# Kernel optimization log

Measured on AMD Instinct MI355X. Metric: run time of the kernel, lower is better.

The kernel has to match this reference:

```python
import jax, jax.numpy as jnp
import numpy as np

N_NODES = 50000
N_EDGES = 1600000
NFEAT = 128
NHID = 128
NCLASS = 64
BATCH = 8


def setup_inputs() -> dict:
    key = jax.random.key(0)
    ks = jax.random.split(key, 8)
    x = jax.random.normal(ks[0], (BATCH, N_NODES, NFEAT), dtype=jnp.float32)
    edge_rows = jnp.sort(jax.random.randint(ks[1], (N_EDGES,), 0, N_NODES))
    edge_cols = jax.random.randint(ks[2], (N_EDGES,), 0, N_NODES)
    # roughly degree-normalized positive weights (avg degree 32)
    edge_vals = jax.random.uniform(ks[3], (N_EDGES,), dtype=jnp.float32) / 32.0
    s1 = 1.0 / np.sqrt(NFEAT)
    W1 = jax.random.normal(ks[4], (NFEAT, NHID), dtype=jnp.float32) * s1
    W2 = jax.random.normal(ks[5], (NHID, NHID), dtype=jnp.float32) * s1
    W3 = jax.random.normal(ks[6], (NHID, NCLASS), dtype=jnp.float32) * s1
    b1 = jnp.zeros((NHID,), dtype=jnp.float32)
    b2 = jnp.zeros((NHID,), dtype=jnp.float32)
    b3 = jnp.zeros((NCLASS,), dtype=jnp.float32)
    return {"x": x, "edge_rows": edge_rows, "edge_cols": edge_cols,
            "edge_vals": edge_vals, "W1": W1, "b1": b1, "W2": W2,
            "b2": b2, "W3": W3, "b3": b3}


def _gcn_layer(x, W, b, rows, cols, vals, n_nodes):
    """Batched SPGraphConvolution: spmm(adj, x @ W) + b, x: [B, N, d_in]."""
    support = jnp.einsum("bnd,de->bne", x, W)  # [B, N, d_out]

    def spmm(s):  # s: [N, d_out]
        msgs = s[cols] * vals[:, None]  # gather + scale, [E, d_out]
        return jax.ops.segment_sum(msgs, rows, num_segments=n_nodes)

    return jax.vmap(spmm)(support) + b


def reference(x, edge_rows, edge_cols, edge_vals, W1, b1, W2, b2, W3, b3):
    n = x.shape[1]
    # dropout in eval mode (training=False) for determinism
    h = jax.nn.relu(_gcn_layer(x, W1, b1, edge_rows, edge_cols, edge_vals, n) + x)
    h = jax.nn.relu(_gcn_layer(h, W2, b2, edge_rows, edge_cols, edge_vals, n) + h)
    h = jax.nn.relu(_gcn_layer(h, W3, b3, edge_rows, edge_cols, edge_vals, n))
    return jax.nn.sigmoid(h)
```

## Files before the change

kernel.cpp:

```cpp
#include <hip/hip_runtime.h>

constexpr int NN = 50000;
constexpr int NE = 1600000;
constexpr int NB = 8;
constexpr int M_ROWS = NN * NB;

typedef unsigned short ushort;
typedef unsigned int uint;
typedef unsigned char uchar;
typedef float f32x2v __attribute__((ext_vector_type(2)));
typedef float f32x4v __attribute__((ext_vector_type(4)));
typedef uint u32x4 __attribute__((ext_vector_type(4)));
typedef uint u32x2 __attribute__((ext_vector_type(2)));

__device__ __forceinline__ ushort f2bf(float f) {
  union { float f; uint u; } v;
  v.f = f;
  const uint r = v.u + 0x7fffu + ((v.u >> 16) & 1u);
  return (ushort)(r >> 16);
}
__device__ __forceinline__ float bfhi(uint g) {
  union { uint u; float f; } v;
  v.u = g & 0xffff0000u;
  return v.f;
}
__device__ __forceinline__ float bflo(uint g) {
  union { uint u; float f; } v;
  v.u = g << 16;
  return v.f;
}

__device__ __forceinline__ void fp8x4_to_f32x2(uint v, f32x2v& lo, f32x2v& hi) {
#if __has_builtin(__builtin_amdgcn_cvt_pk_f32_fp8)
  lo = __builtin_amdgcn_cvt_pk_f32_fp8((int)v, false);
  hi = __builtin_amdgcn_cvt_pk_f32_fp8((int)v, true);
#else
  union { _Float16 h; ushort u; } c0, c1, c2, c3;
  c0.u = (ushort)(((v & 0x80u) << 8) | ((v & 0x7fu) << 7));
  c1.u = (ushort)(((v & 0x8000u)) | ((v & 0x7f00u) >> 1));
  c2.u = (ushort)((((v >> 16) & 0x80u) << 8) | (((v >> 16) & 0x7fu) << 7));
  c3.u = (ushort)((((v >> 24) & 0x80u) << 8) | (((v >> 24) & 0x7fu) << 7));
  lo.x = (float)c0.h * 256.0f;
  lo.y = (float)c1.h * 256.0f;
  hi.x = (float)c2.h * 256.0f;
  hi.y = (float)c3.h * 256.0f;
#endif
}
__device__ __forceinline__ uint f32_to_fp8(float x) {
#if __has_builtin(__builtin_amdgcn_cvt_pk_fp8_f32)
  return (uint)__builtin_amdgcn_cvt_pk_fp8_f32(x, x, 0, false) & 0xffu;
#else
  union { _Float16 h; ushort u; } c;
  c.h = (_Float16)(x * (1.0f / 256.0f));
  const uint h = c.u;
  uint r = h & 0x7fffu;
  r = (r + 0x3Fu + ((r >> 7) & 1u)) >> 7;
  if (r > 0x7Eu) r = 0x7Eu;
  return ((h >> 8) & 0x80u) | r;
#endif
}

__global__ __launch_bounds__(256) void rowptr_kernel(const int* __restrict__ rows,
                                                     int* __restrict__ row_ptr) {
  const int r = blockIdx.x * 256 + threadIdx.x;
  if (r > NN) return;
  int lo = 0, hi = NE;
  while (lo < hi) {
    const int mid = (lo + hi) >> 1;
    if (rows[mid] < r) lo = mid + 1;
    else hi = mid;
  }
  row_ptr[r] = lo;
}

__global__ __launch_bounds__(256) void wtrans_kernel(const float* __restrict__ W,
                                                     ushort* __restrict__ Wt,
                                                     int dout) {
  const int idx = blockIdx.x * 256 + threadIdx.x;
  if (idx >= dout * 128) return;
  const int n = idx >> 7;
  const int k = idx & 127;
  Wt[idx] = f2bf(W[k * dout + n]);
}

template <int DOUT, bool ABF16>
__global__ __launch_bounds__(256) void gemm_mfma(const void* __restrict__ Av,
                                                 const ushort* __restrict__ Wt,
                                                 uchar* __restrict__ S) {
  constexpr int PACK = 256 / DOUT;
  constexpr int NT = DOUT / 16;
  constexpr int RT = 5;
  constexpr int LDK = 136;
  constexpr int LB = DOUT + 16;
  typedef __attribute__((ext_vector_type(8))) short bf16x8;
  typedef __attribute__((ext_vector_type(4))) float f32x4;

  __shared__ ushort As[64 * LDK];
  __shared__ ushort Ws[DOUT * LDK];

  const int t = threadIdx.x;
  const int w = t >> 6;
  const int l = t & 63;

#pragma unroll
  for (int q = 0; q < (DOUT * 128) / (8 * 256); q++) {
    const int chunk = t + q * 256;
    const int n = chunk >> 4;
    const int off = (chunk & 15) * 8;
    *(uint4*)(Ws + n * LDK + off) = *(const uint4*)(Wt + n * 128 + off);
  }

  const int mrow = w * 16 + (l & 15);
  const int q8 = (l >> 4) * 8;

  for (int rt = 0; rt < RT; rt++) {
    const size_t m0 = (size_t)blockIdx.x * (64 * RT) + (size_t)rt * 64;

    if constexpr (ABF16) {
      const ushort* A = (const ushort*)Av;
#pragma unroll
      for (int q = 0; q < 4; q++) {
        const int chunk = t + q * 256;
        const int row = chunk >> 4;
        const int off = (chunk & 15) * 8;
        *(u32x4*)(As + row * LDK + off) =
            __builtin_nontemporal_load((const u32x4*)(A + (m0 + row) * 128 + off));
      }
    } else {
      const float* A = (const float*)Av;
      const int row = t >> 2;
      const int c0 = (t & 3) * 32;
      const float* src = A + (m0 + row) * 128 + c0;
      ushort* dst = As + row * LDK + c0;
#pragma unroll
      for (int q = 0; q < 8; q++) {
        const f32x4v g = __builtin_nontemporal_load((const f32x4v*)(src + q * 4));
        u32x2 p;
        p.x = (uint)f2bf(g.x) | ((uint)f2bf(g.y) << 16);
        p.y = (uint)f2bf(g.z) | ((uint)f2bf(g.w) << 16);
        *(u32x2*)(dst + q * 4) = p;
      }
    }
    __syncthreads();

    bf16x8 a[4];
    const ushort* ap = As + mrow * LDK + q8;
#pragma unroll
    for (int ks = 0; ks < 4; ks++) a[ks] = *(const bf16x8*)(ap + ks * 32);

    f32x4 acc[NT];
#pragma unroll
    for (int nt = 0; nt < NT; nt++) acc[nt] = (f32x4)0.f;

#pragma unroll
    for (int nt = 0; nt < NT; nt++) {
      const ushort* bp = Ws + (nt * 16 + (l & 15)) * LDK + q8;
#pragma unroll
      for (int ks = 0; ks < 4; ks++) {
        const bf16x8 b = *(const bf16x8*)(bp + ks * 32);
        acc[nt] =
            __builtin_amdgcn_mfma_f32_16x16x32_bf16(a[ks], b, acc[nt], 0, 0, 0);
      }
    }

    __syncthreads();
    uchar* Ab = (uchar*)As;
    const int erow = w * 16 + (l >> 4) * 4;
    const int ecol = l & 15;
#pragma unroll
    for (int nt = 0; nt < NT; nt++)
#pragma unroll
      for (int r = 0; r < 4; r++)
        Ab[(erow + r) * LB + nt * 16 + ecol] = (uchar)f32_to_fp8(acc[nt][r]);
    __syncthreads();

#pragma unroll
    for (int q = 0; q < (64 * DOUT) / (16 * 256); q++) {
      const int chunk = t + q * 256;
      const int row = chunk / (DOUT / 16);
      const int off = (chunk % (DOUT / 16)) * 16;
      const uint4 v = *(const uint4*)(Ab + row * LB + off);
      const int m = (int)m0 + row;
      const int b = m / NN;
      const int n = m - b * NN;
      *(uint4*)(S + ((size_t)(b / PACK) * NN + n) * 256 + (b % PACK) * DOUT + off) = v;
    }
    __syncthreads();
  }
}

template <int PACK, int RMODE, bool SIGMOID, bool OBF16>
__global__ __launch_bounds__(256) void spmm_kernel(
    const uchar* __restrict__ S, const int* __restrict__ row_ptr,
    const int* __restrict__ cols, const float* __restrict__ vals,
    const float* __restrict__ bias, const void* resid, void* out) {
  constexpr int DOUT = 256 / PACK;
  constexpr int LPB = 64 / PACK;

  const int wave = threadIdx.x >> 6;
  const int lane = threadIdx.x & 63;
  const int r = __builtin_amdgcn_readfirstlane(blockIdx.x * 4 + wave);
  const int bg = lane / LPB;
  const int j = (lane % LPB) * 4;
  const int b = blockIdx.y * PACK + bg;
  const uchar* __restrict__ Sg = S + (size_t)blockIdx.y * ((size_t)NN * 256);
  const uint lane4 = (uint)lane << 2;

  f32x2v a01 = {0.f, 0.f};
  f32x2v a23 = {0.f, 0.f};

  const int e0 = __builtin_amdgcn_readfirstlane(row_ptr[r]);
  const int e1 = __builtin_amdgcn_readfirstlane(row_ptr[r + 1]);

  int e = e0;
  for (; e + 16 <= e1; e += 16) {
    uint gg[16];
#pragma unroll
    for (int s = 0; s < 16; s++) {
      const uint c8 = ((uint)cols[e + s]) << 8;
      gg[s] = *(const uint*)(Sg + c8 + lane4);
    }
#pragma unroll
    for (int s = 0; s < 16; s++) {
      const float wi = vals[e + s];
      f32x2v lo, hi;
      fp8x4_to_f32x2(gg[s], lo, hi);
      const f32x2v w2 = {wi, wi};
      a01 = __builtin_elementwise_fma(w2, lo, a01);
      a23 = __builtin_elementwise_fma(w2, hi, a23);
    }
  }
  for (; e + 4 <= e1; e += 4) {
    uint gg[4];
#pragma unroll
    for (int s = 0; s < 4; s++) {
      const uint c8 = ((uint)cols[e + s]) << 8;
      gg[s] = *(const uint*)(Sg + c8 + lane4);
    }
#pragma unroll
    for (int s = 0; s < 4; s++) {
      const float wi = vals[e + s];
      f32x2v lo, hi;
      fp8x4_to_f32x2(gg[s], lo, hi);
      const f32x2v w2 = {wi, wi};
      a01 = __builtin_elementwise_fma(w2, lo, a01);
      a23 = __builtin_elementwise_fma(w2, hi, a23);
    }
  }
  for (; e < e1; e++) {
    const uint c8 = ((uint)cols[e]) << 8;
    const float wi = vals[e];
    const uint g = *(const uint*)(Sg + c8 + lane4);
    f32x2v lo, hi;
    fp8x4_to_f32x2(g, lo, hi);
    const f32x2v w2 = {wi, wi};
    a01 = __builtin_elementwise_fma(w2, lo, a01);
    a23 = __builtin_elementwise_fma(w2, hi, a23);
  }

  float a0 = a01.x, a1 = a01.y, a2 = a23.x, a3 = a23.y;

  const size_t orow = (size_t)(b * NN + r) * DOUT + j;
  const f32x4v bb = *(const f32x4v*)(bias + j);
  a0 += bb.x;
  a1 += bb.y;
  a2 += bb.z;
  a3 += bb.w;
  if constexpr (RMODE == 1) {
    const f32x4v res =
        __builtin_nontemporal_load((const f32x4v*)((const float*)resid + orow));
    a0 += res.x;
    a1 += res.y;
    a2 += res.z;
    a3 += res.w;
  } else if constexpr (RMODE == 2) {
    const u32x2 g =
        __builtin_nontemporal_load((const u32x2*)((const ushort*)resid + orow));
    a0 += bflo(g.x);
    a1 += bfhi(g.x);
    a2 += bflo(g.y);
    a3 += bfhi(g.y);
  }
  a0 = fmaxf(a0, 0.f);
  a1 = fmaxf(a1, 0.f);
  a2 = fmaxf(a2, 0.f);
  a3 = fmaxf(a3, 0.f);
  if constexpr (SIGMOID) {
    a0 = 1.f / (1.f + __expf(-a0));
    a1 = 1.f / (1.f + __expf(-a1));
    a2 = 1.f / (1.f + __expf(-a2));
    a3 = 1.f / (1.f + __expf(-a3));
  }
  if constexpr (OBF16) {
    u32x2 o;
    o.x = (uint)f2bf(a0) | ((uint)f2bf(a1) << 16);
    o.y = (uint)f2bf(a2) | ((uint)f2bf(a3) << 16);
    __builtin_nontemporal_store(o, (u32x2*)((ushort*)out + orow));
  } else {
    f32x4v o;
    o.x = a0;
    o.y = a1;
    o.z = a2;
    o.w = a3;
    __builtin_nontemporal_store(o, (f32x4v*)((float*)out + orow));
  }
}

extern "C" void kernel_launch(void* const* d_in, const int* in_sizes, int n_in,
                              void* d_out, int out_size, void* d_ws, size_t ws_size,
                              hipStream_t stream) {
  const float* x = (const float*)d_in[0];
  const int* erows = (const int*)d_in[1];
  const int* ecols = (const int*)d_in[2];
  const float* evals = (const float*)d_in[3];
  const float* W1 = (const float*)d_in[4];
  const float* b1 = (const float*)d_in[5];
  const float* W2 = (const float*)d_in[6];
  const float* b2 = (const float*)d_in[7];
  const float* W3 = (const float*)d_in[8];
  const float* b3 = (const float*)d_in[9];

  char* ws = (char*)d_ws;
  int* row_ptr = (int*)ws;
  ushort* Wt1 = (ushort*)(ws + 0x40000);
  ushort* Wt2 = (ushort*)(ws + 0x48000);
  ushort* Wt3 = (ushort*)(ws + 0x50000);
  uchar* Sf8 = (uchar*)(ws + 0x60000);
  ushort* H = (ushort*)(ws + 0x60000 + (size_t)M_ROWS * 128);

  rowptr_kernel<<<(NN + 256) / 256, 256, 0, stream>>>(erows, row_ptr);
  wtrans_kernel<<<(128 * 128) / 256, 256, 0, stream>>>(W1, Wt1, 128);
  wtrans_kernel<<<(128 * 128) / 256, 256, 0, stream>>>(W2, Wt2, 128);
  wtrans_kernel<<<(64 * 128) / 256, 256, 0, stream>>>(W3, Wt3, 64);

  const dim3 sgrid128(NN / 4, NB / 2);
  const dim3 sgrid64(NN / 4, NB / 4);
  constexpr int GB = M_ROWS / (64 * 5);

  gemm_mfma<128, false><<<GB, 256, 0, stream>>>(x, Wt1, Sf8);
  spmm_kernel<2, 1, false, true><<<sgrid128, 256, 0, stream>>>(
      Sf8, row_ptr, ecols, evals, b1, x, H);
  gemm_mfma<128, true><<<GB, 256, 0, stream>>>(H, Wt2, Sf8);
  spmm_kernel<2, 2, false, true><<<sgrid128, 256, 0, stream>>>(
      Sf8, row_ptr, ecols, evals, b2, H, H);
  gemm_mfma<64, true><<<GB, 256, 0, stream>>>(H, Wt3, Sf8);
  spmm_kernel<4, 0, true, false><<<sgrid64, 256, 0, stream>>>(
      Sf8, row_ptr, ecols, evals, b3, nullptr, (float*)d_out);
}
```

Before: 930.4 us.

## Store fp8 support in 64-byte column slabs and split edges across wave quarters

The GEMM now writes the fp8 support matrix as column slabs of 64 bytes per node instead of 256-byte packed rows. The SpMM is restructured so each wave's four 16-lane quarters handle different edges of the same row, using vector loads of cols and vals, and the partial sums are combined with cross-lane shuffles. Blocks are ordered so that 8 slices are processed in phases, aiming to keep each slab's working set (about 3.2 MB) resident in cache and to raise memory-level parallelism. The costs are more launched blocks, repeated reads of row_ptr, cols and vals once per slice, and shuffle overhead.

```diff
diff --git a/kernel.cpp b/kernel.cpp
--- a/kernel.cpp
+++ b/kernel.cpp
@@ -4,6 +4,7 @@
 constexpr int NE = 1600000;
 constexpr int NB = 8;
 constexpr int M_ROWS = NN * NB;
+constexpr int SLAB = NN * 64;
 
 typedef unsigned short ushort;
 typedef unsigned int uint;
@@ -12,6 +13,8 @@
 typedef float f32x4v __attribute__((ext_vector_type(4)));
 typedef uint u32x4 __attribute__((ext_vector_type(4)));
 typedef uint u32x2 __attribute__((ext_vector_type(2)));
+typedef uint u32x4a __attribute__((ext_vector_type(4), aligned(4)));
+typedef float f32x4a __attribute__((ext_vector_type(4), aligned(4)));
 
 __device__ __forceinline__ ushort f2bf(float f) {
   union { float f; uint u; } v;
@@ -87,7 +90,6 @@
 __global__ __launch_bounds__(256) void gemm_mfma(const void* __restrict__ Av,
                                                  const ushort* __restrict__ Wt,
                                                  uchar* __restrict__ S) {
-  constexpr int PACK = 256 / DOUT;
   constexpr int NT = DOUT / 16;
   constexpr int RT = 5;
   constexpr int LDK = 136;
@@ -183,28 +185,34 @@
       const int m = (int)m0 + row;
       const int b = m / NN;
       const int n = m - b * NN;
-      *(uint4*)(S + ((size_t)(b / PACK) * NN + n) * 256 + (b % PACK) * DOUT + off) = v;
+      const int gcol = b * DOUT + off;
+      *(uint4*)(S + (size_t)(gcol >> 6) * SLAB + (size_t)n * 64 + (gcol & 63)) = v;
     }
     __syncthreads();
   }
 }
 
-template <int PACK, int RMODE, bool SIGMOID, bool OBF16>
-__global__ __launch_bounds__(256) void spmm_kernel(
+template <int SLICES, int SPB, int RMODE, bool SIGMOID, bool OBF16>
+__global__ __launch_bounds__(256) void spmm_sliced(
     const uchar* __restrict__ S, const int* __restrict__ row_ptr,
     const int* __restrict__ cols, const float* __restrict__ vals,
     const float* __restrict__ bias, const void* resid, void* out) {
-  constexpr int DOUT = 256 / PACK;
-  constexpr int LPB = 64 / PACK;
+  constexpr int D = SPB * 64;
+  constexpr int PER_PHASE = (NN / 4) * 8;
 
   const int wave = threadIdx.x >> 6;
   const int lane = threadIdx.x & 63;
-  const int r = __builtin_amdgcn_readfirstlane(blockIdx.x * 4 + wave);
-  const int bg = lane / LPB;
-  const int j = (lane % LPB) * 4;
-  const int b = blockIdx.y * PACK + bg;
-  const uchar* __restrict__ Sg = S + (size_t)blockIdx.y * ((size_t)NN * 256);
-  const uint lane4 = (uint)lane << 2;
+  const int q = lane >> 4;
+  const int qi = lane & 15;
+
+  const int bid = blockIdx.x;
+  const int phase = bid / PER_PHASE;
+  const int within = bid - phase * PER_PHASE;
+  const int slice = phase * 8 + (within & 7);
+  const int rc = within >> 3;
+  const int r = __builtin_amdgcn_readfirstlane(rc * 4 + wave);
+
+  const uint vbase = (uint)slice * (uint)SLAB + (uint)(qi * 4);
 
   f32x2v a01 = {0.f, 0.f};
   f32x2v a23 = {0.f, 0.f};
@@ -214,95 +222,101 @@
 
   int e = e0;
   for (; e + 16 <= e1; e += 16) {
-    uint gg[16];
-#pragma unroll
-    for (int s = 0; s < 16; s++) {
-      const uint c8 = ((uint)cols[e + s]) << 8;
-      gg[s] = *(const uint*)(Sg + c8 + lane4);
-    }
-#pragma unroll
-    for (int s = 0; s < 16; s++) {
-      const float wi = vals[e + s];
+    const int eq = e + q * 4;
+    const u32x4a cc = *(const u32x4a*)(cols + eq);
+    const f32x4a ww = *(const f32x4a*)(vals + eq);
+    uint g0 = *(const uint*)(S + ((cc.x << 6) + vbase));
+    uint g1 = *(const uint*)(S + ((cc.y << 6) + vbase));
+    uint g2 = *(const uint*)(S + ((cc.z << 6) + vbase));
+    uint g3 = *(const uint*)(S + ((cc.w << 6) + vbase));
+    f32x2v lo, hi;
+    fp8x4_to_f32x2(g0, lo, hi);
+    f32x2v w2 = {ww.x, ww.x};
+    a01 = __builtin_elementwise_fma(w2, lo, a01);
+    a23 = __builtin_elementwise_fma(w2, hi, a23);
+    fp8x4_to_f32x2(g1, lo, hi);
+    w2.x = ww.y; w2.y = ww.y;
+    a01 = __builtin_elementwise_fma(w2, lo, a01);
+    a23 = __builtin_elementwise_fma(w2, hi, a23);
+    fp8x4_to_f32x2(g2, lo, hi);
+    w2.x = ww.z; w2.y = ww.z;
+    a01 = __builtin_elementwise_fma(w2, lo, a01);
+    a23 = __builtin_elementwise_fma(w2, hi, a23);
+    fp8x4_to_f32x2(g3, lo, hi);
+    w2.x = ww.w; w2.y = ww.w;
+    a01 = __builtin_elementwise_fma(w2, lo, a01);
+    a23 = __builtin_elementwise_fma(w2, hi, a23);
+  }
+  if (e < e1) {
+    const int eqt = e + q * 4;
+#pragma unroll
+    for (int k = 0; k < 4; k++) {
+      const int idx = eqt + k;
+      const int cidx = idx < e1 ? idx : e1 - 1;
+      const uint cv = (uint)cols[cidx];
+      const float wk = idx < e1 ? vals[cidx] : 0.f;
+      const uint g = *(const uint*)(S + ((cv << 6) + vbase));
       f32x2v lo, hi;
-      fp8x4_to_f32x2(gg[s], lo, hi);
-      const f32x2v w2 = {wi, wi};
+      fp8x4_to_f32x2(g, lo, hi);
+      const f32x2v w2 = {wk, wk};
       a01 = __builtin_elementwise_fma(w2, lo, a01);
       a23 = __builtin_elementwise_fma(w2, hi, a23);
     }
   }
-  for (; e + 4 <= e1; e += 4) {
-    uint gg[4];
-#pragma unroll
-    for (int s = 0; s < 4; s++) {
-      const uint c8 = ((uint)cols[e + s]) << 8;
-      gg[s] = *(const uint*)(Sg + c8 + lane4);
-    }
-#pragma unroll
-    for (int s = 0; s < 4; s++) {
-      const float wi = vals[e + s];
-      f32x2v lo, hi;
-      fp8x4_to_f32x2(gg[s], lo, hi);
-      const f32x2v w2 = {wi, wi};
-      a01 = __builtin_elementwise_fma(w2, lo, a01);
-      a23 = __builtin_elementwise_fma(w2, hi, a23);
-    }
-  }
-  for (; e < e1; e++) {
-    const uint c8 = ((uint)cols[e]) << 8;
-    const float wi = vals[e];
-    const uint g = *(const uint*)(Sg + c8 + lane4);
-    f32x2v lo, hi;
-    fp8x4_to_f32x2(g, lo, hi);
-    const f32x2v w2 = {wi, wi};
-    a01 = __builtin_elementwise_fma(w2, lo, a01);
-    a23 = __builtin_elementwise_fma(w2, hi, a23);
-  }
 
   float a0 = a01.x, a1 = a01.y, a2 = a23.x, a3 = a23.y;
-
-  const size_t orow = (size_t)(b * NN + r) * DOUT + j;
-  const f32x4v bb = *(const f32x4v*)(bias + j);
-  a0 += bb.x;
-  a1 += bb.y;
-  a2 += bb.z;
-  a3 += bb.w;
-  if constexpr (RMODE == 1) {
-    const f32x4v res =
-        __builtin_nontemporal_load((const f32x4v*)((const float*)resid + orow));
-    a0 += res.x;
-    a1 += res.y;
-    a2 += res.z;
-    a3 += res.w;
-  } else if constexpr (RMODE == 2) {
-    const u32x2 g =
-        __builtin_nontemporal_load((const u32x2*)((const ushort*)resid + orow));
-    a0 += bflo(g.x);
-    a1 += bfhi(g.x);
-    a2 += bflo(g.y);
-    a3 += bfhi(g.y);
-  }
-  a0 = fmaxf(a0, 0.f);
-  a1 = fmaxf(a1, 0.f);
-  a2 = fmaxf(a2, 0.f);
-  a3 = fmaxf(a3, 0.f);
-  if constexpr (SIGMOID) {
-    a0 = 1.f / (1.f + __expf(-a0));
-    a1 = 1.f / (1.f + __expf(-a1));
-    a2 = 1.f / (1.f + __expf(-a2));
-    a3 = 1.f / (1.f + __expf(-a3));
-  }
-  if constexpr (OBF16) {
-    u32x2 o;
-    o.x = (uint)f2bf(a0) | ((uint)f2bf(a1) << 16);
-    o.y = (uint)f2bf(a2) | ((uint)f2bf(a3) << 16);
-    __builtin_nontemporal_store(o, (u32x2*)((ushort*)out + orow));
-  } else {
-    f32x4v o;
-    o.x = a0;
-    o.y = a1;
-    o.z = a2;
-    o.w = a3;
-    __builtin_nontemporal_store(o, (f32x4v*)((float*)out + orow));
+  a0 += __shfl_xor(a0, 16); a0 += __shfl_xor(a0, 32);
+  a1 += __shfl_xor(a1, 16); a1 += __shfl_xor(a1, 32);
+  a2 += __shfl_xor(a2, 16); a2 += __shfl_xor(a2, 32);
+  a3 += __shfl_xor(a3, 16); a3 += __shfl_xor(a3, 32);
+
+  if (q == 0) {
+    const int b = slice / SPB;
+    const int f0 = (slice - b * SPB) * 64 + qi * 4;
+    const size_t orow = ((size_t)b * NN + r) * D + f0;
+    const f32x4v bb = *(const f32x4v*)(bias + f0);
+    a0 += bb.x;
+    a1 += bb.y;
+    a2 += bb.z;
+    a3 += bb.w;
+    if constexpr (RMODE == 1) {
+      const f32x4v res =
+          __builtin_nontemporal_load((const f32x4v*)((const float*)resid + orow));
+      a0 += res.x;
+      a1 += res.y;
+      a2 += res.z;
+      a3 += res.w;
+    } else if constexpr (RMODE == 2) {
+      const u32x2 g =
+          __builtin_nontemporal_load((const u32x2*)((const ushort*)resid + orow));
+      a0 += bflo(g.x);
+      a1 += bfhi(g.x);
+      a2 += bflo(g.y);
+      a3 += bfhi(g.y);
+    }
+    a0 = fmaxf(a0, 0.f);
+    a1 = fmaxf(a1, 0.f);
+    a2 = fmaxf(a2, 0.f);
+    a3 = fmaxf(a3, 0.f);
+    if constexpr (SIGMOID) {
+      a0 = 1.f / (1.f + __expf(-a0));
+      a1 = 1.f / (1.f + __expf(-a1));
+      a2 = 1.f / (1.f + __expf(-a2));
+      a3 = 1.f / (1.f + __expf(-a3));
+    }
+    if constexpr (OBF16) {
+      u32x2 o;
+      o.x = (uint)f2bf(a0) | ((uint)f2bf(a1) << 16);
+      o.y = (uint)f2bf(a2) | ((uint)f2bf(a3) << 16);
+      __builtin_nontemporal_store(o, (u32x2*)((ushort*)out + orow));
+    } else {
+      f32x4v o;
+      o.x = a0;
+      o.y = a1;
+      o.z = a2;
+      o.w = a3;
+      __builtin_nontemporal_store(o, (f32x4v*)((float*)out + orow));
+    }
   }
 }
 
@@ -333,17 +347,15 @@
   wtrans_kernel<<<(128 * 128) / 256, 256, 0, stream>>>(W2, Wt2, 128);
   wtrans_kernel<<<(64 * 128) / 256, 256, 0, stream>>>(W3, Wt3, 64);
 
-  const dim3 sgrid128(NN / 4, NB / 2);
-  const dim3 sgrid64(NN / 4, NB / 4);
   constexpr int GB = M_ROWS / (64 * 5);
 
   gemm_mfma<128, false><<<GB, 256, 0, stream>>>(x, Wt1, Sf8);
-  spmm_kernel<2, 1, false, true><<<sgrid128, 256, 0, stream>>>(
+  spmm_sliced<16, 2, 1, false, true><<<(NN / 4) * 16, 256, 0, stream>>>(
       Sf8, row_ptr, ecols, evals, b1, x, H);
   gemm_mfma<128, true><<<GB, 256, 0, stream>>>(H, Wt2, Sf8);
-  spmm_kernel<2, 2, false, true><<<sgrid128, 256, 0, stream>>>(
+  spmm_sliced<16, 2, 2, false, true><<<(NN / 4) * 16, 256, 0, stream>>>(
       Sf8, row_ptr, ecols, evals, b2, H, H);
   gemm_mfma<64, true><<<GB, 256, 0, stream>>>(H, Wt3, Sf8);
-  spmm_kernel<4, 0, true, false><<<sgrid64, 256, 0, stream>>>(
+  spmm_sliced<8, 1, 0, true, false><<<(NN / 4) * 8, 256, 0, stream>>>(
       Sf8, row_ptr, ecols, evals, b3, nullptr, (float*)d_out);
 }
```

Measured after the change: 1.502 ms. 1.61x slower.
